# Kernel optimization log

Hardware: AMD Instinct MI355X
Metric: run time of the kernel (lower is better)

## Reference

```python
import jax, jax.numpy as jnp
import numpy as np

B, N = 16, 131072
C_MID, C_OUT = 128, 16


def setup_inputs() -> dict:
    key = jax.random.key(0)
    k1, k2, k3, k4 = jax.random.split(key, 4)
    # points in roughly [-0.5, 0.5] so cube indexing covers the grids
    x = jax.random.uniform(k1, (B, N, 3), dtype=jnp.float32) - 0.5
    W1 = jax.random.normal(k2, (C_MID, 3), dtype=jnp.float32) * 0.1
    b1 = jnp.zeros((C_MID,), jnp.float32)
    W2 = jax.random.normal(k3, (C_OUT, C_MID), dtype=jnp.float32) * 0.1
    b2 = jnp.zeros((C_OUT,), jnp.float32)
    # fixed per-batch permutations (deterministic stand-in for torch.randperm)
    perm = jnp.stack([jax.random.permutation(jax.random.fold_in(k4, i), N)
                      for i in range(B)]).astype(jnp.int32)
    return {"x": x, "W1": W1, "b1": b1, "W2": W2, "b2": b2, "perm": perm}


def point_to_cell(pts, feat, W, H, D):
    # pts float [B,N,3] already clamped to [0, dim-1]; cast like torch LongTensor
    idx = pts.astype(jnp.int32)
    flat = (idx[..., 0] * H + idx[..., 1]) * D + idx[..., 2]  # [B,N]
    Bb, Nn, C = feat.shape

    def scatter_one(fi, fe):
        grid = jnp.zeros((W * H * D, C), feat.dtype)
        return grid.at[fi].set(fe)

    cell = jax.vmap(scatter_one)(flat, feat)           # [B, WHD, C]
    return cell.transpose(0, 2, 1).reshape(Bb, C, W, H, D)


def reference(x, W1, b1, W2, b2, perm):
    # PointNetfeatLocal: 1x1 Conv1d stack == per-point MLP 3 -> 128 -> 16
    h = jnp.maximum(jnp.einsum('bnc,hc->bnh', x, W1) + b1, 0.0)
    feat = jnp.einsum('bnh,oh->bno', h, W2) + b2       # [B,N,16]
    # shuffle_points_feat: per-batch permutation gather
    xs = jnp.take_along_axis(x, perm[..., None], axis=1)
    fs = jnp.take_along_axis(feat, perm[..., None], axis=1)
    # batch_grid_pooling32 / 64
    cube32 = jnp.clip(xs * 32.0 + 16.5, 0.0, 31.0)
    cube64 = jnp.clip(xs * 64.0 + 32.5, 0.0, 63.0)
    feat_cell32 = point_to_cell(cube32, fs, 32, 32, 32)  # [B,16,32,32,32]
    feat_cell64 = point_to_cell(cube64, fs, 64, 64, 64)  # [B,16,64,64,64]
    return feat_cell32, feat_cell64
```

## Files before the change

kernel.cpp:

```cpp
#include <hip/hip_runtime.h>

namespace {
constexpr int kB = 16;
constexpr int kN = 131072;
constexpr int kNLog = 17;
constexpr int kCMid = 128;
constexpr int kCOut = 16;
constexpr int kCells32Log = 15;
constexpr int kCells64Log = 18;
constexpr int kCells32 = 1 << kCells32Log;
constexpr int kCells64 = 1 << kCells64Log;
constexpr long kOut32Elems = (long)kB * kCOut * kCells32;
constexpr int kChunks32 = 16;
constexpr int kSlabs64 = 16;
constexpr int kSlabCells = kCells64 / kSlabs64;
}

__device__ inline unsigned int packbf2(float lo, float hi) {
    unsigned int a = __float_as_uint(lo);
    unsigned int b = __float_as_uint(hi);
    a = (a + 0x7FFFu + ((a >> 16) & 1u)) >> 16;
    b = (b + 0x7FFFu + ((b >> 16) & 1u)) & 0xFFFF0000u;
    return b | a;
}
__device__ inline float bf_lo(unsigned int p) { return __uint_as_float(p << 16); }
__device__ inline float bf_hi(unsigned int p) { return __uint_as_float(p & 0xFFFF0000u); }

__global__ __launch_bounds__(256) void k_pack(
    const float* __restrict__ W1, const float* __restrict__ b1,
    const float* __restrict__ W2,
    float* __restrict__ W1p, float* __restrict__ W2t)
{
    const int t = threadIdx.x;
    for (int k = t; k < kCMid; k += 256) {
        W1p[k * 4 + 0] = W1[k * 3 + 0];
        W1p[k * 4 + 1] = W1[k * 3 + 1];
        W1p[k * 4 + 2] = W1[k * 3 + 2];
        W1p[k * 4 + 3] = b1[k];
    }
    for (int idx = t; idx < kCOut * kCMid; idx += 256) {
        const int c = idx >> 7;
        const int k = idx & 127;
        W2t[k * kCOut + c] = W2[idx];
    }
}

__global__ __launch_bounds__(256) void k_prec(
    const float* __restrict__ x,
    const int* __restrict__ perm,
    unsigned long long* __restrict__ prec)
{
    const long gid = (long)blockIdx.x * 256 + threadIdx.x;
    const long bbase = gid & ~(long)(kN - 1);
    const int i = (int)(gid & (kN - 1));
    const int j = perm[gid];

    const float* xp = x + (bbase + j) * 3;
    const float v0 = xp[0], v1 = xp[1], v2 = xp[2];

    const int ix32 = (int)fminf(fmaxf(__fadd_rn(__fmul_rn(v0, 32.0f), 16.5f), 0.0f), 31.0f);
    const int iy32 = (int)fminf(fmaxf(__fadd_rn(__fmul_rn(v1, 32.0f), 16.5f), 0.0f), 31.0f);
    const int iz32 = (int)fminf(fmaxf(__fadd_rn(__fmul_rn(v2, 32.0f), 16.5f), 0.0f), 31.0f);
    const int ix64 = (int)fminf(fmaxf(__fadd_rn(__fmul_rn(v0, 64.0f), 32.5f), 0.0f), 63.0f);
    const int iy64 = (int)fminf(fmaxf(__fadd_rn(__fmul_rn(v1, 64.0f), 32.5f), 0.0f), 63.0f);
    const int iz64 = (int)fminf(fmaxf(__fadd_rn(__fmul_rn(v2, 64.0f), 32.5f), 0.0f), 63.0f);

    const unsigned long long cell32 = (unsigned long long)((ix32 * 32 + iy32) * 32 + iz32);
    const unsigned long long cell64 = (unsigned long long)((ix64 * 64 + iy64) * 64 + iz64);
    prec[bbase + j] = (cell64 << 33) | (cell32 << 18) | (unsigned long long)(i + 1);
}

__global__ __launch_bounds__(256, 4) void k_mlp(
    const float* __restrict__ x,
    const float* __restrict__ W1p, const float* __restrict__ W2t,
    const float* __restrict__ b2,
    uint4* __restrict__ feat)
{
    const long pair = (long)blockIdx.x * 256 + threadIdx.x;
    const long p0 = pair * 2;

    const float2 xa = *(const float2*)(x + p0 * 3 + 0);
    const float2 xb = *(const float2*)(x + p0 * 3 + 2);
    const float2 xc = *(const float2*)(x + p0 * 3 + 4);
    const float x00 = xa.x, x01 = xa.y, x02 = xb.x;
    const float x10 = xb.y, x11 = xc.x, x12 = xc.y;

    float acc0[kCOut], acc1[kCOut];
    #pragma unroll
    for (int c = 0; c < kCOut; ++c) { acc0[c] = 0.0f; acc1[c] = 0.0f; }

    const float4* __restrict__ w1v = (const float4*)W1p;
    const float4* __restrict__ w2v = (const float4*)W2t;

    #pragma unroll 4
    for (int k = 0; k < kCMid; ++k) {
        const float4 w1 = w1v[k];
        const float h0 = fmaxf(fmaf(w1.x, x00, fmaf(w1.y, x01, fmaf(w1.z, x02, w1.w))), 0.0f);
        const float h1 = fmaxf(fmaf(w1.x, x10, fmaf(w1.y, x11, fmaf(w1.z, x12, w1.w))), 0.0f);
        #pragma unroll
        for (int q = 0; q < 4; ++q) {
            const float4 wq = w2v[k * 4 + q];
            acc0[4 * q + 0] = fmaf(wq.x, h0, acc0[4 * q + 0]);
            acc0[4 * q + 1] = fmaf(wq.y, h0, acc0[4 * q + 1]);
            acc0[4 * q + 2] = fmaf(wq.z, h0, acc0[4 * q + 2]);
            acc0[4 * q + 3] = fmaf(wq.w, h0, acc0[4 * q + 3]);
            acc1[4 * q + 0] = fmaf(wq.x, h1, acc1[4 * q + 0]);
            acc1[4 * q + 1] = fmaf(wq.y, h1, acc1[4 * q + 1]);
            acc1[4 * q + 2] = fmaf(wq.z, h1, acc1[4 * q + 2]);
            acc1[4 * q + 3] = fmaf(wq.w, h1, acc1[4 * q + 3]);
        }
    }

    const float4 bq0 = ((const float4*)b2)[0];
    const float4 bq1 = ((const float4*)b2)[1];
    const float4 bq2 = ((const float4*)b2)[2];
    const float4 bq3 = ((const float4*)b2)[3];

    uint4 f;
    f.x = packbf2(acc0[0]  + bq0.x, acc0[1]  + bq0.y);
    f.y = packbf2(acc0[2]  + bq0.z, acc0[3]  + bq0.w);
    f.z = packbf2(acc0[4]  + bq1.x, acc0[5]  + bq1.y);
    f.w = packbf2(acc0[6]  + bq1.z, acc0[7]  + bq1.w);
    feat[p0 * 2 + 0] = f;
    f.x = packbf2(acc0[8]  + bq2.x, acc0[9]  + bq2.y);
    f.y = packbf2(acc0[10] + bq2.z, acc0[11] + bq2.w);
    f.z = packbf2(acc0[12] + bq3.x, acc0[13] + bq3.y);
    f.w = packbf2(acc0[14] + bq3.z, acc0[15] + bq3.w);
    feat[p0 * 2 + 1] = f;
    f.x = packbf2(acc1[0]  + bq0.x, acc1[1]  + bq0.y);
    f.y = packbf2(acc1[2]  + bq0.z, acc1[3]  + bq0.w);
    f.z = packbf2(acc1[4]  + bq1.x, acc1[5]  + bq1.y);
    f.w = packbf2(acc1[6]  + bq1.z, acc1[7]  + bq1.w);
    feat[p0 * 2 + 2] = f;
    f.x = packbf2(acc1[8]  + bq2.x, acc1[9]  + bq2.y);
    f.y = packbf2(acc1[10] + bq2.z, acc1[11] + bq2.w);
    f.z = packbf2(acc1[12] + bq3.x, acc1[13] + bq3.y);
    f.w = packbf2(acc1[14] + bq3.z, acc1[15] + bq3.w);
    feat[p0 * 2 + 3] = f;
}

__global__ __launch_bounds__(1024) void k_win32(
    const unsigned long long* __restrict__ prec,
    unsigned int* __restrict__ partial32)
{
    __shared__ unsigned int lwin[kCells32];
    const int b = blockIdx.x >> 4;
    const int c = blockIdx.x & (kChunks32 - 1);
    const int t = threadIdx.x;

    #pragma unroll
    for (int r = 0; r < kCells32 / 1024; ++r) lwin[r * 1024 + t] = 0u;
    __syncthreads();

    const long base = ((long)b << kNLog) + (long)c * (kN / kChunks32);
    #pragma unroll
    for (int r = 0; r < (kN / kChunks32) / 1024; ++r) {
        const unsigned long long w = prec[base + r * 1024 + t];
        atomicMax(&lwin[(int)((w >> 18) & 0x7FFFull)], (unsigned int)(w & 0x3FFFFull));
    }
    __syncthreads();

    unsigned int* dst = partial32 + ((long)blockIdx.x << kCells32Log);
    #pragma unroll
    for (int r = 0; r < kCells32 / 1024; ++r) dst[r * 1024 + t] = lwin[r * 1024 + t];
}

__global__ __launch_bounds__(1024) void k_win64(
    const unsigned long long* __restrict__ prec,
    unsigned long long* __restrict__ win64)
{
    __shared__ unsigned long long lwin[kSlabCells];
    const int b = blockIdx.x >> 4;
    const int s = blockIdx.x & (kSlabs64 - 1);
    const int t = threadIdx.x;

    #pragma unroll
    for (int r = 0; r < kSlabCells / 1024; ++r) lwin[r * 1024 + t] = 0ull;
    __syncthreads();

    const long base = (long)b << kNLog;
    for (int r = 0; r < kN / 1024; ++r) {
        const int j = r * 1024 + t;
        const unsigned long long w = prec[base + j];
        const int cell = (int)(w >> 33);
        if ((cell >> 14) == s)
            atomicMax(&lwin[cell & (kSlabCells - 1)],
                      ((w & 0x3FFFFull) << 32) | (unsigned long long)(unsigned int)j);
    }
    __syncthreads();

    unsigned long long* dst = win64 + ((long)b << kCells64Log) + ((long)s << 14);
    #pragma unroll
    for (int r = 0; r < kSlabCells / 1024; ++r) dst[r * 1024 + t] = lwin[r * 1024 + t];
}

__global__ __launch_bounds__(256) void k_gather32(
    const unsigned int* __restrict__ partial32,
    const int* __restrict__ perm,
    const uint4* __restrict__ feat,
    float* __restrict__ out)
{
    const long gid = (long)blockIdx.x * 256 + threadIdx.x;
    const int b = (int)(gid >> kCells32Log);
    const int cell = (int)(gid & (kCells32 - 1));

    unsigned int w = 0u;
    #pragma unroll
    for (int c = 0; c < kChunks32; ++c)
        w = max(w, partial32[(((long)(b * kChunks32 + c)) << kCells32Log) + cell]);

    float v[kCOut];
    #pragma unroll
    for (int c = 0; c < kCOut; ++c) v[c] = 0.0f;

    if (w != 0u) {
        const int i = (int)(w - 1u);
        const int j = perm[((long)b << kNLog) + i];
        const long pidx = ((long)b << kNLog) + j;
        const uint4 f0 = feat[pidx * 2 + 0];
        const uint4 f1 = feat[pidx * 2 + 1];
        v[0]  = bf_lo(f0.x); v[1]  = bf_hi(f0.x);
        v[2]  = bf_lo(f0.y); v[3]  = bf_hi(f0.y);
        v[4]  = bf_lo(f0.z); v[5]  = bf_hi(f0.z);
        v[6]  = bf_lo(f0.w); v[7]  = bf_hi(f0.w);
        v[8]  = bf_lo(f1.x); v[9]  = bf_hi(f1.x);
        v[10] = bf_lo(f1.y); v[11] = bf_hi(f1.y);
        v[12] = bf_lo(f1.z); v[13] = bf_hi(f1.z);
        v[14] = bf_lo(f1.w); v[15] = bf_hi(f1.w);
    }

    float* op = out + (((long)b * kCOut) << kCells32Log) + cell;
    #pragma unroll
    for (int c = 0; c < kCOut; ++c) op[(long)c << kCells32Log] = v[c];
}

__global__ __launch_bounds__(256) void k_gather64(
    const unsigned long long* __restrict__ win,
    const uint4* __restrict__ feat,
    float* __restrict__ out)
{
    const long gid = (long)blockIdx.x * 256 + threadIdx.x;
    const int b = (int)(gid >> kCells64Log);
    const int cell = (int)(gid & (kCells64 - 1));
    const unsigned long long w = win[gid];

    float v[kCOut];
    #pragma unroll
    for (int c = 0; c < kCOut; ++c) v[c] = 0.0f;

    if (w != 0ull) {
        const int j = (int)(w & 0xFFFFFFFFull);
        const long pidx = ((long)b << kNLog) + j;
        const uint4 f0 = feat[pidx * 2 + 0];
        const uint4 f1 = feat[pidx * 2 + 1];
        v[0]  = bf_lo(f0.x); v[1]  = bf_hi(f0.x);
        v[2]  = bf_lo(f0.y); v[3]  = bf_hi(f0.y);
        v[4]  = bf_lo(f0.z); v[5]  = bf_hi(f0.z);
        v[6]  = bf_lo(f0.w); v[7]  = bf_hi(f0.w);
        v[8]  = bf_lo(f1.x); v[9]  = bf_hi(f1.x);
        v[10] = bf_lo(f1.y); v[11] = bf_hi(f1.y);
        v[12] = bf_lo(f1.z); v[13] = bf_hi(f1.z);
        v[14] = bf_lo(f1.w); v[15] = bf_hi(f1.w);
    }

    float* op = out + (((long)b * kCOut) << kCells64Log) + cell;
    #pragma unroll
    for (int c = 0; c < kCOut; ++c) op[(long)c << kCells64Log] = v[c];
}

extern "C" void kernel_launch(void* const* d_in, const int* in_sizes, int n_in,
                              void* d_out, int out_size, void* d_ws, size_t ws_size,
                              hipStream_t stream)
{
    const float* x  = (const float*)d_in[0];
    const float* W1 = (const float*)d_in[1];
    const float* b1 = (const float*)d_in[2];
    const float* W2 = (const float*)d_in[3];
    const float* b2 = (const float*)d_in[4];
    const int* perm = (const int*)d_in[5];

    float* out32 = (float*)d_out;
    float* out64 = out32 + kOut32Elems;

    float* W1p = (float*)d_ws;
    float* W2t = W1p + kCMid * 4;
    unsigned long long* prec = (unsigned long long*)((char*)d_ws + 16384);
    unsigned int* partial32 = (unsigned int*)(prec + (size_t)kB * kN);
    unsigned long long* win64 =
        (unsigned long long*)(partial32 + (size_t)kB * kChunks32 * kCells32);
    uint4* feat = (uint4*)(win64 + (size_t)kB * kCells64);

    const int nPtsBlocks  = (int)(((long)kB * kN) / 256);
    const int nPairBlocks = (int)(((long)kB * kN) / 512);
    const int n32Blocks   = (int)(((long)kB * kCells32) / 256);
    const int n64Blocks   = (int)(((long)kB * kCells64) / 256);
    dim3 blk(256);

    k_pack<<<1, 256, 0, stream>>>(W1, b1, W2, W1p, W2t);
    k_prec<<<nPtsBlocks, blk, 0, stream>>>(x, perm, prec);
    k_mlp<<<nPairBlocks, blk, 0, stream>>>(x, W1p, W2t, b2, feat);

    k_win32<<<kB * kChunks32, 1024, 0, stream>>>(prec, partial32);
    k_win64<<<kB * kSlabs64, 1024, 0, stream>>>(prec, win64);

    k_gather32<<<n32Blocks, blk, 0, stream>>>(partial32, perm, feat, out32);
    k_gather64<<<n64Blocks, blk, 0, stream>>>(win64, feat, out64);
}
```

Baseline: 315.9 us.

## Compute second MLP layer with bf16 MFMA using split hi/lo precision

Replaces the scalar FMA second-layer matmul (128->16) with MFMA 16x16x32 bf16 instructions. Precision is kept with a three-term split, hi*hi + hi*lo + lo*hi, applied to both the weights and the hidden activations. W2 is pre-packed into hi/lo bf16 fragments in the pack kernel, and each wave now processes 64 points. The aim is to cut the VALU FMA cost of the MLP, in exchange for extra packing work and an approximation of fp32 accuracy.

```diff
diff --git a/kernel.cpp b/kernel.cpp
--- a/kernel.cpp
+++ b/kernel.cpp
@@ -16,6 +16,9 @@
 constexpr int kSlabCells = kCells64 / kSlabs64;
 }
 
+typedef __bf16 bf16x8 __attribute__((ext_vector_type(8)));
+typedef float f32x4 __attribute__((ext_vector_type(4)));
+
 __device__ inline unsigned int packbf2(float lo, float hi) {
     unsigned int a = __float_as_uint(lo);
     unsigned int b = __float_as_uint(hi);
@@ -26,10 +29,17 @@
 __device__ inline float bf_lo(unsigned int p) { return __uint_as_float(p << 16); }
 __device__ inline float bf_hi(unsigned int p) { return __uint_as_float(p & 0xFFFF0000u); }
 
+__device__ inline uint4 pack8(const float* h) {
+    uint4 r;
+    r.x = packbf2(h[0], h[1]); r.y = packbf2(h[2], h[3]);
+    r.z = packbf2(h[4], h[5]); r.w = packbf2(h[6], h[7]);
+    return r;
+}
+
 __global__ __launch_bounds__(256) void k_pack(
     const float* __restrict__ W1, const float* __restrict__ b1,
     const float* __restrict__ W2,
-    float* __restrict__ W1p, float* __restrict__ W2t)
+    float* __restrict__ W1p, uint4* __restrict__ w2h, uint4* __restrict__ w2l)
 {
     const int t = threadIdx.x;
     for (int k = t; k < kCMid; k += 256) {
@@ -38,10 +48,22 @@
         W1p[k * 4 + 2] = W1[k * 3 + 2];
         W1p[k * 4 + 3] = b1[k];
     }
-    for (int idx = t; idx < kCOut * kCMid; idx += 256) {
-        const int c = idx >> 7;
-        const int k = idx & 127;
-        W2t[k * kCOut + c] = W2[idx];
+    {
+        const int kw = t >> 6;
+        const int lane = t & 63;
+        const int ch = lane & 15;
+        const int grp = lane >> 4;
+        float v[8], lo[8];
+        #pragma unroll
+        for (int e = 0; e < 8; ++e)
+            v[e] = W2[ch * kCMid + kw * 32 + grp * 8 + e];
+        const uint4 hh = pack8(v);
+        lo[0] = v[0] - bf_lo(hh.x); lo[1] = v[1] - bf_hi(hh.x);
+        lo[2] = v[2] - bf_lo(hh.y); lo[3] = v[3] - bf_hi(hh.y);
+        lo[4] = v[4] - bf_lo(hh.z); lo[5] = v[5] - bf_hi(hh.z);
+        lo[6] = v[6] - bf_lo(hh.w); lo[7] = v[7] - bf_hi(hh.w);
+        w2h[t] = hh;
+        w2l[t] = pack8(lo);
     }
 }
 
@@ -72,71 +94,73 @@
 
 __global__ __launch_bounds__(256, 4) void k_mlp(
     const float* __restrict__ x,
-    const float* __restrict__ W1p, const float* __restrict__ W2t,
+    const float* __restrict__ W1p,
+    const uint4* __restrict__ w2h, const uint4* __restrict__ w2l,
     const float* __restrict__ b2,
-    uint4* __restrict__ feat)
-{
-    const long pair = (long)blockIdx.x * 256 + threadIdx.x;
-    const long p0 = pair * 2;
-
-    const float2 xa = *(const float2*)(x + p0 * 3 + 0);
-    const float2 xb = *(const float2*)(x + p0 * 3 + 2);
-    const float2 xc = *(const float2*)(x + p0 * 3 + 4);
-    const float x00 = xa.x, x01 = xa.y, x02 = xb.x;
-    const float x10 = xb.y, x11 = xc.x, x12 = xc.y;
-
-    float acc0[kCOut], acc1[kCOut];
-    #pragma unroll
-    for (int c = 0; c < kCOut; ++c) { acc0[c] = 0.0f; acc1[c] = 0.0f; }
+    uint2* __restrict__ feat)
+{
+    const int tid = threadIdx.x;
+    const int lane = tid & 63;
+    const int grp = lane >> 4;
+    const int pt16 = lane & 15;
+    const long base = (((long)blockIdx.x << 2) + (tid >> 6)) << 6;
+
+    float xv[4][3];
+    #pragma unroll
+    for (int t = 0; t < 4; ++t) {
+        const float* xp = x + (base + t * 16 + pt16) * 3;
+        xv[t][0] = xp[0]; xv[t][1] = xp[1]; xv[t][2] = xp[2];
+    }
+
+    f32x4 acc[4];
+    #pragma unroll
+    for (int t = 0; t < 4; ++t) acc[t] = (f32x4){0.f, 0.f, 0.f, 0.f};
 
     const float4* __restrict__ w1v = (const float4*)W1p;
-    const float4* __restrict__ w2v = (const float4*)W2t;
-
-    #pragma unroll 4
-    for (int k = 0; k < kCMid; ++k) {
-        const float4 w1 = w1v[k];
-        const float h0 = fmaxf(fmaf(w1.x, x00, fmaf(w1.y, x01, fmaf(w1.z, x02, w1.w))), 0.0f);
-        const float h1 = fmaxf(fmaf(w1.x, x10, fmaf(w1.y, x11, fmaf(w1.z, x12, w1.w))), 0.0f);
+
+    #pragma unroll
+    for (int kw = 0; kw < 4; ++kw) {
+        const bf16x8 ah = __builtin_bit_cast(bf16x8, w2h[(kw << 6) + lane]);
+        const bf16x8 al = __builtin_bit_cast(bf16x8, w2l[(kw << 6) + lane]);
+        float4 w1r[8];
         #pragma unroll
-        for (int q = 0; q < 4; ++q) {
-            const float4 wq = w2v[k * 4 + q];
-            acc0[4 * q + 0] = fmaf(wq.x, h0, acc0[4 * q + 0]);
-            acc0[4 * q + 1] = fmaf(wq.y, h0, acc0[4 * q + 1]);
-            acc0[4 * q + 2] = fmaf(wq.z, h0, acc0[4 * q + 2]);
-            acc0[4 * q + 3] = fmaf(wq.w, h0, acc0[4 * q + 3]);
-            acc1[4 * q + 0] = fmaf(wq.x, h1, acc1[4 * q + 0]);
-            acc1[4 * q + 1] = fmaf(wq.y, h1, acc1[4 * q + 1]);
-            acc1[4 * q + 2] = fmaf(wq.z, h1, acc1[4 * q + 2]);
-            acc1[4 * q + 3] = fmaf(wq.w, h1, acc1[4 * q + 3]);
+        for (int e = 0; e < 8; ++e)
+            w1r[e] = w1v[(kw << 5) + (grp << 3) + e];
+
+        #pragma unroll
+        for (int t = 0; t < 4; ++t) {
+            float h[8], lo[8];
+            #pragma unroll
+            for (int e = 0; e < 8; ++e)
+                h[e] = fmaxf(fmaf(w1r[e].x, xv[t][0],
+                              fmaf(w1r[e].y, xv[t][1],
+                               fmaf(w1r[e].z, xv[t][2], w1r[e].w))), 0.0f);
+            const uint4 bh = pack8(h);
+            lo[0] = h[0] - bf_lo(bh.x); lo[1] = h[1] - bf_hi(bh.x);
+            lo[2] = h[2] - bf_lo(bh.y); lo[3] = h[3] - bf_hi(bh.y);
+            lo[4] = h[4] - bf_lo(bh.z); lo[5] = h[5] - bf_hi(bh.z);
+            lo[6] = h[6] - bf_lo(bh.w); lo[7] = h[7] - bf_hi(bh.w);
+            const uint4 bl4 = pack8(lo);
+            const bf16x8 bhv = __builtin_bit_cast(bf16x8, bh);
+            const bf16x8 blv = __builtin_bit_cast(bf16x8, bl4);
+            acc[t] = __builtin_amdgcn_mfma_f32_16x16x32_bf16(ah, bhv, acc[t], 0, 0, 0);
+            acc[t] = __builtin_amdgcn_mfma_f32_16x16x32_bf16(ah, blv, acc[t], 0, 0, 0);
+            acc[t] = __builtin_amdgcn_mfma_f32_16x16x32_bf16(al, bhv, acc[t], 0, 0, 0);
         }
     }
 
-    const float4 bq0 = ((const float4*)b2)[0];
-    const float4 bq1 = ((const float4*)b2)[1];
-    const float4 bq2 = ((const float4*)b2)[2];
-    const float4 bq3 = ((const float4*)b2)[3];
-
-    uint4 f;
-    f.x = packbf2(acc0[0]  + bq0.x, acc0[1]  + bq0.y);
-    f.y = packbf2(acc0[2]  + bq0.z, acc0[3]  + bq0.w);
-    f.z = packbf2(acc0[4]  + bq1.x, acc0[5]  + bq1.y);
-    f.w = packbf2(acc0[6]  + bq1.z, acc0[7]  + bq1.w);
-    feat[p0 * 2 + 0] = f;
-    f.x = packbf2(acc0[8]  + bq2.x, acc0[9]  + bq2.y);
-    f.y = packbf2(acc0[10] + bq2.z, acc0[11] + bq2.w);
-    f.z = packbf2(acc0[12] + bq3.x, acc0[13] + bq3.y);
-    f.w = packbf2(acc0[14] + bq3.z, acc0[15] + bq3.w);
-    feat[p0 * 2 + 1] = f;
-    f.x = packbf2(acc1[0]  + bq0.x, acc1[1]  + bq0.y);
-    f.y = packbf2(acc1[2]  + bq0.z, acc1[3]  + bq0.w);
-    f.z = packbf2(acc1[4]  + bq1.x, acc1[5]  + bq1.y);
-    f.w = packbf2(acc1[6]  + bq1.z, acc1[7]  + bq1.w);
-    feat[p0 * 2 + 2] = f;
-    f.x = packbf2(acc1[8]  + bq2.x, acc1[9]  + bq2.y);
-    f.y = packbf2(acc1[10] + bq2.z, acc1[11] + bq2.w);
-    f.z = packbf2(acc1[12] + bq3.x, acc1[13] + bq3.y);
-    f.w = packbf2(acc1[14] + bq3.z, acc1[15] + bq3.w);
-    feat[p0 * 2 + 3] = f;
+    const float4 bias = ((const float4*)b2)[grp];
+    #pragma unroll
+    for (int t = 0; t < 4; ++t) {
+        const float c0 = acc[t][0] + bias.x;
+        const float c1 = acc[t][1] + bias.y;
+        const float c2 = acc[t][2] + bias.z;
+        const float c3 = acc[t][3] + bias.w;
+        uint2 o;
+        o.x = packbf2(c0, c1);
+        o.y = packbf2(c2, c3);
+        feat[((base + t * 16 + pt16) << 2) + grp] = o;
+    }
 }
 
 __global__ __launch_bounds__(1024) void k_win32(
@@ -283,22 +307,22 @@
     float* out64 = out32 + kOut32Elems;
 
     float* W1p = (float*)d_ws;
-    float* W2t = W1p + kCMid * 4;
+    uint4* w2h = (uint4*)((char*)d_ws + 2048);
+    uint4* w2l = w2h + 256;
     unsigned long long* prec = (unsigned long long*)((char*)d_ws + 16384);
     unsigned int* partial32 = (unsigned int*)(prec + (size_t)kB * kN);
     unsigned long long* win64 =
         (unsigned long long*)(partial32 + (size_t)kB * kChunks32 * kCells32);
     uint4* feat = (uint4*)(win64 + (size_t)kB * kCells64);
 
-    const int nPtsBlocks  = (int)(((long)kB * kN) / 256);
-    const int nPairBlocks = (int)(((long)kB * kN) / 512);
-    const int n32Blocks   = (int)(((long)kB * kCells32) / 256);
-    const int n64Blocks   = (int)(((long)kB * kCells64) / 256);
+    const int nPtsBlocks = (int)(((long)kB * kN) / 256);
+    const int n32Blocks  = (int)(((long)kB * kCells32) / 256);
+    const int n64Blocks  = (int)(((long)kB * kCells64) / 256);
     dim3 blk(256);
 
-    k_pack<<<1, 256, 0, stream>>>(W1, b1, W2, W1p, W2t);
+    k_pack<<<1, 256, 0, stream>>>(W1, b1, W2, W1p, w2h, w2l);
     k_prec<<<nPtsBlocks, blk, 0, stream>>>(x, perm, prec);
-    k_mlp<<<nPairBlocks, blk, 0, stream>>>(x, W1p, W2t, b2, feat);
+    k_mlp<<<nPtsBlocks, blk, 0, stream>>>(x, W1p, w2h, w2l, b2, (uint2*)feat);
 
     k_win32<<<kB * kChunks32, 1024, 0, stream>>>(prec, partial32);
     k_win64<<<kB * kSlabs64, 1024, 0, stream>>>(prec, win64);
```

Measured after the change: 299.0 us. 5.3% less time.
